# Kernel tuning notes

Measured on AMD Instinct MI355X. Metric: run time of the kernel, lower is better.

The kernel has to match this reference:

```python
import jax, jax.numpy as jnp
import numpy as np
import math

N_EMBD = 1024
N_HEAD = 16
HEAD_DIM = N_EMBD // N_HEAD


def setup_inputs() -> dict:
    key = jax.random.key(0)
    k_x, k_w1, k_b1, k_w2, k_b2 = jax.random.split(key, 5)
    B, T = 2, 2048
    x = jax.random.normal(k_x, (B, T, N_EMBD), dtype=jnp.float32)
    # ln1: Linear(n_embd, 3*n_embd); weights stored as [in, out] for x @ W
    W_qkv = jax.random.normal(k_w1, (N_EMBD, 3 * N_EMBD), dtype=jnp.float32) * 0.02
    b_qkv = jax.random.normal(k_b1, (3 * N_EMBD,), dtype=jnp.float32) * 0.02
    # ln2: Linear(n_embd, n_embd)
    W_out = jax.random.normal(k_w2, (N_EMBD, N_EMBD), dtype=jnp.float32) * 0.02
    b_out = jax.random.normal(k_b2, (N_EMBD,), dtype=jnp.float32) * 0.02
    return {"x": x, "W_qkv": W_qkv, "b_qkv": b_qkv, "W_out": W_out, "b_out": b_out}


def reference(x, W_qkv, b_qkv, W_out, b_out):
    B, T, C = x.shape
    qkv = x @ W_qkv + b_qkv                      # [B,T,3C]
    q, k, v = jnp.split(qkv, 3, axis=-1)
    # reshape to heads: [B, H, T, D]
    def to_heads(t):
        return t.reshape(B, T, N_HEAD, HEAD_DIM).transpose(0, 2, 1, 3)
    Q, K, V = to_heads(q), to_heads(k), to_heads(v)
    # NOTE: scale is 1/sqrt(n_head), as in the source (not sqrt(head_dim));
    # NOTE: no causal mask is applied, faithfully matching the source forward.
    scale = 1.0 / math.sqrt(N_HEAD)
    scores = jnp.einsum('bhqd,bhkd->bhqk', Q, K) * scale  # [B,H,T,T]
    attn = jax.nn.softmax(scores, axis=-1)
    out = jnp.einsum('bhqk,bhkd->bhqd', attn, V)          # [B,H,T,D]
    out = out.transpose(0, 2, 1, 3).reshape(B, T, C)
    # dropout = 0.0 -> identity (eval mode)
    return out @ W_out + b_out
```

## Files before the change

kernel.cpp:

```cpp
#include <hip/hip_runtime.h>
#include <hip/hip_bf16.h>
#include <stdint.h>

typedef __bf16 bf16_t;
typedef __bf16 bf16x8 __attribute__((ext_vector_type(8)));
typedef float  f32x4  __attribute__((ext_vector_type(4)));

#define AS1 __attribute__((address_space(1)))
#define AS3 __attribute__((address_space(3)))

__device__ __forceinline__ void gload16(const bf16_t* g, char* l) {
  __builtin_amdgcn_global_load_lds((AS1 const void*)(uintptr_t)g, (AS3 void*)l, 16, 0, 0);
}
__device__ __forceinline__ int swz8(int r) { return (r & 7) ^ ((r >> 2) & 6); }

#define C2S 0.36067376022224085f

__global__ __launch_bounds__(256) void prep(
    const float* __restrict__ x, const float* __restrict__ Wqkv, const float* __restrict__ Wout,
    bf16_t* __restrict__ xb, bf16_t* __restrict__ wqkvT, bf16_t* __restrict__ woutT) {
  __shared__ float tile[32][33];
  const int bid = blockIdx.x, tid = threadIdx.x;
  if (bid < 4096) {
    const int i = bid * 256 + tid;
    float4 v = reinterpret_cast<const float4*>(x)[i];
    union { bf16_t h[4]; unsigned long long u; } r;
    r.h[0] = (bf16_t)v.x; r.h[1] = (bf16_t)v.y; r.h[2] = (bf16_t)v.z; r.h[3] = (bf16_t)v.w;
    reinterpret_cast<unsigned long long*>(xb)[i] = r.u;
    return;
  }
  const float* W; bf16_t* Wt; int N, tb;
  if (bid < 7168) { W = Wqkv; Wt = wqkvT; N = 3072; tb = bid - 4096; }
  else            { W = Wout; Wt = woutT; N = 1024; tb = bid - 7168; }
  const int kb = (tb & 31) * 32, nb = (tb >> 5) * 32;
  const int tx = tid & 31, ty = tid >> 5;
#pragma unroll
  for (int i = 0; i < 32; i += 8)
    tile[ty + i][tx] = W[(size_t)(kb + ty + i) * N + nb + tx];
  __syncthreads();
#pragma unroll
  for (int i = 0; i < 32; i += 8)
    Wt[(size_t)(nb + ty + i) * 1024 + kb + tx] = (bf16_t)tile[tx][ty + i];
}

template<int MI>
__global__ __launch_bounds__(256) void gemm_bt(
    const bf16_t* __restrict__ A, const bf16_t* __restrict__ Bt,
    const float* __restrict__ bias,
    bf16_t* __restrict__ outb, bf16_t* __restrict__ vtb, float* __restrict__ outf,
    int M, int N, int K, int ldo, int mode) {
  __shared__ bf16_t lA[3][MI * 1024];
  __shared__ bf16_t lB[3][4096];
  const int tid = threadIdx.x;
  const int wave = tid >> 6, lane = tid & 63;
  const int lr = lane & 15, lg = lane >> 4;
  const int ntiles = N >> 7;
  const int bid = (blockIdx.x & 7) * ((int)gridDim.x >> 3) + (blockIdx.x >> 3);
  const int bn = bid % ntiles, bm = bid / ntiles;
  const int m0 = bm * (MI * 32), n0 = bn * 128;
  const int wr = wave >> 1, wc = wave & 1;
  f32x4 acc[MI][4] = {};

  auto stageg = [&](int buf, int k0) {
#pragma unroll
    for (int it = 0; it < MI / 2; ++it) {
      const int wbase = it * 256 + wave * 64;
      const int lam = wbase + lane;
      const int row = lam >> 2;
      const int colb = ((lam & 3) << 4) ^ (((row >> 1) & 3) << 4);
      gload16(A + (size_t)(m0 + row) * K + k0 + (colb >> 1), (char*)&lA[buf][0] + wbase * 16);
    }
#pragma unroll
    for (int it = 0; it < 2; ++it) {
      const int wbase = it * 256 + wave * 64;
      const int lam = wbase + lane;
      const int row = lam >> 2;
      const int colb = ((lam & 3) << 4) ^ (((row >> 1) & 3) << 4);
      gload16(Bt + (size_t)(n0 + row) * K + k0 + (colb >> 1), (char*)&lB[buf][0] + wbase * 16);
    }
  };

  const int nt = K >> 5;
  stageg(0, 0);
  stageg(1, 32);
  int cur = 0, stg = 2;

  for (int t = 0; t < nt; ++t) {
    if (t + 2 < nt) stageg(stg, (t + 2) << 5);
    if (t + 2 < nt) {
      if constexpr (MI == 4) asm volatile("s_waitcnt vmcnt(8)" ::: "memory");
      else                   asm volatile("s_waitcnt vmcnt(6)" ::: "memory");
    } else if (t + 1 < nt) {
      if constexpr (MI == 4) asm volatile("s_waitcnt vmcnt(4)" ::: "memory");
      else                   asm volatile("s_waitcnt vmcnt(3)" ::: "memory");
    } else {
      asm volatile("s_waitcnt vmcnt(0)" ::: "memory");
    }
    __builtin_amdgcn_s_barrier();
    __builtin_amdgcn_sched_barrier(0);

    const char* pA = (const char*)&lA[cur][0];
    const char* pB = (const char*)&lB[cur][0];
    bf16x8 af[MI], bfv[4];
#pragma unroll
    for (int mi = 0; mi < MI; ++mi) {
      const int row = wr * (MI * 16) + mi * 16 + lr;
      af[mi] = *reinterpret_cast<const bf16x8*>(
          pA + row * 64 + ((lg * 16) ^ (((row >> 1) & 3) << 4)));
    }
#pragma unroll
    for (int ni = 0; ni < 4; ++ni) {
      const int row = wc * 64 + ni * 16 + lr;
      bfv[ni] = *reinterpret_cast<const bf16x8*>(
          pB + row * 64 + ((lg * 16) ^ (((row >> 1) & 3) << 4)));
    }
    __builtin_amdgcn_s_setprio(1);
#pragma unroll
    for (int mi = 0; mi < MI; ++mi)
#pragma unroll
      for (int ni = 0; ni < 4; ++ni)
        acc[mi][ni] = __builtin_amdgcn_mfma_f32_16x16x32_bf16(af[mi], bfv[ni], acc[mi][ni], 0, 0, 0);
    __builtin_amdgcn_s_setprio(0);

    __builtin_amdgcn_sched_barrier(0);
    __builtin_amdgcn_s_barrier();
    cur = cur == 2 ? 0 : cur + 1;
    stg = stg == 2 ? 0 : stg + 1;
  }

#pragma unroll
  for (int mi = 0; mi < MI; ++mi) {
#pragma unroll
    for (int ni = 0; ni < 4; ++ni) {
      const int col = n0 + wc * 64 + ni * 16 + lr;
      const float bv = bias[col];
      const int rg0 = m0 + wr * (MI * 16) + mi * 16 + lg * 4;
      if (mode == 1 && col >= 2048) {
        const int colv = col - 2048;
        const int dd = colv & 63, hh = colv >> 6;
        const int bb = rg0 >> 11, t = rg0 & 2047;
        union { bf16_t h4[4]; unsigned long long u; } pk;
#pragma unroll
        for (int r = 0; r < 4; ++r) pk.h4[r] = (bf16_t)(acc[mi][ni][r] + bv);
        *reinterpret_cast<unsigned long long*>(
            vtb + (size_t)(bb * 16 + hh) * 131072 + (size_t)dd * 2048 + t) = pk.u;
      } else {
        const float sc = (mode == 1 && col < 1024) ? C2S : 1.f;
#pragma unroll
        for (int r = 0; r < 4; ++r) {
          const float v = (acc[mi][ni][r] + bv) * sc;
          if (mode == 2) outf[(size_t)(rg0 + r) * ldo + col] = v;
          else           outb[(size_t)(rg0 + r) * ldo + col] = (bf16_t)v;
        }
      }
    }
  }
}

__global__ __launch_bounds__(512) void attn_fwd(
    const bf16_t* __restrict__ qkv2,
    const bf16_t* __restrict__ vT,
    bf16_t* __restrict__ a0, bf16_t* __restrict__ a1,
    float* __restrict__ lbuf) {
  __shared__ bf16_t lds[3][8192];
  const int tid = threadIdx.x;
  const int wave = tid >> 6, lane = tid & 63;
  const int lr = lane & 15, lg = lane >> 4;
  const int id = blockIdx.x;
  const int xcd = id & 7, slot = id >> 3;
  const int bh = xcd * 4 + (slot & 3);
  const int rest = slot >> 2;
  const int qb = rest & 7, kvh = rest >> 3;
  const int b = bh >> 4, h = bh & 15;

  const int q0 = qb * 256 + wave * 32;
  const bf16_t* Qp = qkv2 + (size_t)(b * 2048 + q0) * 2048 + h * 64;
  bf16x8 qf[2][2];
#pragma unroll
  for (int hx = 0; hx < 2; ++hx) {
    qf[hx][0] = *reinterpret_cast<const bf16x8*>(Qp + (size_t)(hx * 16 + lr) * 2048 + lg * 8);
    qf[hx][1] = *reinterpret_cast<const bf16x8*>(Qp + (size_t)(hx * 16 + lr) * 2048 + 32 + lg * 8);
  }

  const int kr = tid >> 3;
  const int ks = (tid & 7) ^ swz8(kr);
  const bf16_t* Ksrc = qkv2 + (size_t)(b * 2048 + kvh * 1024 + kr) * 2048 + 1024 + h * 64 + ks * 8;
  const bf16_t* Vsrc = vT + (size_t)bh * 131072 + (size_t)kr * 2048 + kvh * 1024 + ks * 8;

  auto stage = [&](int buf, int kb) {
    char* base = (char*)&lds[buf][0] + wave * 1024;
    gload16(Ksrc + (size_t)kb * 131072, base);
    gload16(Vsrc + (size_t)kb * 64, base + 8192);
  };

  int kofs[4][2], vofs[4][2];
#pragma unroll
  for (int t = 0; t < 4; ++t) {
    const int kk = 32 * (t >> 1) + 8 * (lr >> 2) + 4 * (t & 1) + (lr & 3);
    const int sw = swz8(kk) << 4;
    kofs[t][0] = (kk << 7) + ((lg * 16) ^ sw);
    kofs[t][1] = (kk << 7) + ((64 + lg * 16) ^ sw);
  }
#pragma unroll
  for (int nc = 0; nc < 4; ++nc) {
    const int vr = nc * 16 + lr;
    const int sw = swz8(vr) << 4;
    vofs[nc][0] = 8192 + (vr << 7) + ((lg * 16) ^ sw);
    vofs[nc][1] = 8192 + (vr << 7) + ((64 + lg * 16) ^ sw);
  }

  f32x4 acc[2][4] = {};
  f32x4 accl[2] = {};
  bf16x8 ones;
#pragma unroll
  for (int j = 0; j < 8; ++j) ones[j] = (bf16_t)1.0f;

  stage(0, 0);
  stage(1, 1);
  int cur = 0, stg = 2;

  for (int kb = 0; kb < 16; ++kb) {
    if (kb + 2 < 16) stage(stg, kb + 2);
    if (kb + 2 < 16)      asm volatile("s_waitcnt vmcnt(4)" ::: "memory");
    else if (kb + 1 < 16) asm volatile("s_waitcnt vmcnt(2)" ::: "memory");
    else                  asm volatile("s_waitcnt vmcnt(0)" ::: "memory");
    __builtin_amdgcn_s_barrier();
    __builtin_amdgcn_sched_barrier(0);
    const char* bK = (const char*)&lds[cur][0];

    f32x4 s[2][4];
#pragma unroll
    for (int t = 0; t < 4; ++t) {
      const bf16x8 k0 = *reinterpret_cast<const bf16x8*>(bK + kofs[t][0]);
      const bf16x8 k1 = *reinterpret_cast<const bf16x8*>(bK + kofs[t][1]);
#pragma unroll
      for (int hx = 0; hx < 2; ++hx) {
        f32x4 z = {0.f, 0.f, 0.f, 0.f};
        z = __builtin_amdgcn_mfma_f32_16x16x32_bf16(k0, qf[hx][0], z, 0, 0, 0);
        s[hx][t] = __builtin_amdgcn_mfma_f32_16x16x32_bf16(k1, qf[hx][1], z, 0, 0, 0);
      }
    }

    bf16x8 pa[2][2];
#pragma unroll
    for (int hx = 0; hx < 2; ++hx) {
      float p[16];
#pragma unroll
      for (int t = 0; t < 4; ++t)
#pragma unroll
        for (int r = 0; r < 4; ++r)
          p[t * 4 + r] = __builtin_amdgcn_exp2f(s[hx][t][r]);
#pragma unroll
      for (int j = 0; j < 8; ++j) { pa[hx][0][j] = (bf16_t)p[j]; pa[hx][1][j] = (bf16_t)p[8 + j]; }
    }

    __builtin_amdgcn_s_setprio(1);
#pragma unroll
    for (int hx = 0; hx < 2; ++hx) {
      accl[hx] = __builtin_amdgcn_mfma_f32_16x16x32_bf16(pa[hx][0], ones, accl[hx], 0, 0, 0);
      accl[hx] = __builtin_amdgcn_mfma_f32_16x16x32_bf16(pa[hx][1], ones, accl[hx], 0, 0, 0);
    }

#pragma unroll
    for (int nc = 0; nc < 4; ++nc) {
      const bf16x8 v0 = *reinterpret_cast<const bf16x8*>(bK + vofs[nc][0]);
      const bf16x8 v1 = *reinterpret_cast<const bf16x8*>(bK + vofs[nc][1]);
#pragma unroll
      for (int hx = 0; hx < 2; ++hx) {
        acc[hx][nc] = __builtin_amdgcn_mfma_f32_16x16x32_bf16(pa[hx][0], v0, acc[hx][nc], 0, 0, 0);
        acc[hx][nc] = __builtin_amdgcn_mfma_f32_16x16x32_bf16(pa[hx][1], v1, acc[hx][nc], 0, 0, 0);
      }
    }
    __builtin_amdgcn_s_setprio(0);

    __builtin_amdgcn_sched_barrier(0);
    __builtin_amdgcn_s_barrier();
    cur = cur == 2 ? 0 : cur + 1;
    stg = stg == 2 ? 0 : stg + 1;
  }

  bf16_t* ap = kvh ? a1 : a0;
#pragma unroll
  for (int hx = 0; hx < 2; ++hx) {
#pragma unroll
    for (int r = 0; r < 4; ++r) {
      const float lf = 1.f / accl[hx][r];
      const int qg = q0 + hx * 16 + lg * 4 + r;
      bf16_t* op = ap + (size_t)(b * 2048 + qg) * 1024 + h * 64 + lr;
#pragma unroll
      for (int nc = 0; nc < 4; ++nc) op[nc * 16] = (bf16_t)(acc[hx][nc][r] * lf);
      if (lr == 0)
        lbuf[(size_t)(kvh * 4096 + b * 2048 + qg) * 16 + h] = accl[hx][r];
    }
  }
}

__global__ void attn_reduce(const bf16_t* __restrict__ a0, const bf16_t* __restrict__ a1,
                            const float* __restrict__ lbuf, bf16_t* __restrict__ aout) {
  const int i = blockIdx.x * 256 + threadIdx.x;
  const int r = i >> 7, h = (i & 127) >> 3;
  const float l0 = lbuf[(size_t)r * 16 + h];
  const float l1 = lbuf[(size_t)(4096 + r) * 16 + h];
  const float inv = 1.f / (l0 + l1);
  const float w0 = l0 * inv, w1 = l1 * inv;
  const bf16x8 v0 = reinterpret_cast<const bf16x8*>(a0)[i];
  const bf16x8 v1 = reinterpret_cast<const bf16x8*>(a1)[i];
  bf16x8 o;
#pragma unroll
  for (int j = 0; j < 8; ++j) o[j] = (bf16_t)(w0 * (float)v0[j] + w1 * (float)v1[j]);
  reinterpret_cast<bf16x8*>(aout)[i] = o;
}

extern "C" void kernel_launch(void* const* d_in, const int* in_sizes, int n_in,
                              void* d_out, int out_size, void* d_ws, size_t ws_size,
                              hipStream_t stream) {
  (void)in_sizes; (void)n_in; (void)out_size; (void)ws_size;
  const float* x    = (const float*)d_in[0];
  const float* Wqkv = (const float*)d_in[1];
  const float* bqkv = (const float*)d_in[2];
  const float* Wout = (const float*)d_in[3];
  const float* bout = (const float*)d_in[4];
  float* out = (float*)d_out;

  char* ws = (char*)d_ws;
  bf16_t* xb    = (bf16_t*)(ws);
  bf16_t* a0    = (bf16_t*)(ws);
  bf16_t* wqkvT = (bf16_t*)(ws + 8388608);
  bf16_t* woutT = (bf16_t*)(ws + 14680064);
  bf16_t* qkv2  = (bf16_t*)(ws + 16777216);
  bf16_t* aout  = (bf16_t*)(ws + 16777216);
  bf16_t* vT    = (bf16_t*)(ws + 33554432);
  bf16_t* a1    = (bf16_t*)(ws + 41943040);
  float*  lbuf  = (float*)(ws + 50331648);

  prep<<<8192, 256, 0, stream>>>(x, Wqkv, Wout, xb, wqkvT, woutT);
  gemm_bt<4><<<768, 256, 0, stream>>>(xb, wqkvT, bqkv, qkv2, vT, nullptr, 4096, 3072, 1024, 2048, 1);
  attn_fwd<<<512, 512, 0, stream>>>(qkv2, vT, a0, a1, lbuf);
  attn_reduce<<<2048, 256, 0, stream>>>(a0, a1, lbuf, aout);
  gemm_bt<2><<<512, 256, 0, stream>>>(aout, woutT, bout, nullptr, nullptr, out, 4096, 1024, 1024, 1024, 2);
}
```

Measured before the change: 113.9 us.

## Interleave GEMM LDS reads, global prefetch and MFMA in barrier-separated phases

Restructures the GEMM main loop into phases. Each phase issues a few LDS fragment reads and one slice of the next-tile global-to-LDS prefetch, then a barrier and lgkmcnt wait, then a batch of MFMAs. The aim is to overlap LDS traffic and global loads with matrix math instead of issuing all prefetches and reads ahead of the compute block. The vmcnt waits are adjusted to the new issue order, and more barriers per k-step are added, which adds synchronisation overhead and risks stalls.

```diff
diff --git a/kernel.cpp b/kernel.cpp
--- a/kernel.cpp
+++ b/kernel.cpp
@@ -15,6 +15,8 @@
 __device__ __forceinline__ int swz8(int r) { return (r & 7) ^ ((r >> 2) & 6); }
 
 #define C2S 0.36067376022224085f
+#define LGKM0 do { asm volatile("s_waitcnt lgkmcnt(0)" ::: "memory"); \
+                   __builtin_amdgcn_sched_barrier(0); } while (0)
 
 __global__ __launch_bounds__(256) void prep(
     const float* __restrict__ x, const float* __restrict__ Wqkv, const float* __restrict__ Wout,
@@ -61,23 +63,30 @@
   const int wr = wave >> 1, wc = wave & 1;
   f32x4 acc[MI][4] = {};
 
+  const int lamw = wave * 64 + lane;
+  const int srow = lamw >> 2;
+  const int scolb = ((lamw & 3) << 4) ^ (((srow >> 1) & 3) << 4);
+  auto stageA = [&](int buf, int k0, int it) {
+    gload16(A + (size_t)(m0 + it * 64 + srow) * K + k0 + (scolb >> 1),
+            (char*)&lA[buf][0] + (it * 256 + wave * 64) * 16);
+  };
+  auto stageB = [&](int buf, int k0, int it) {
+    gload16(Bt + (size_t)(n0 + it * 64 + srow) * K + k0 + (scolb >> 1),
+            (char*)&lB[buf][0] + (it * 256 + wave * 64) * 16);
+  };
   auto stageg = [&](int buf, int k0) {
 #pragma unroll
-    for (int it = 0; it < MI / 2; ++it) {
-      const int wbase = it * 256 + wave * 64;
-      const int lam = wbase + lane;
-      const int row = lam >> 2;
-      const int colb = ((lam & 3) << 4) ^ (((row >> 1) & 3) << 4);
-      gload16(A + (size_t)(m0 + row) * K + k0 + (colb >> 1), (char*)&lA[buf][0] + wbase * 16);
-    }
-#pragma unroll
-    for (int it = 0; it < 2; ++it) {
-      const int wbase = it * 256 + wave * 64;
-      const int lam = wbase + lane;
-      const int row = lam >> 2;
-      const int colb = ((lam & 3) << 4) ^ (((row >> 1) & 3) << 4);
-      gload16(Bt + (size_t)(n0 + row) * K + k0 + (colb >> 1), (char*)&lB[buf][0] + wbase * 16);
-    }
+    for (int it = 0; it < MI / 2; ++it) stageA(buf, k0, it);
+    stageB(buf, k0, 0); stageB(buf, k0, 1);
+  };
+
+  auto ldA = [&](const char* p, int mi) {
+    const int row = wr * (MI * 16) + mi * 16 + lr;
+    return *reinterpret_cast<const bf16x8*>(p + row * 64 + ((lg * 16) ^ (((row >> 1) & 3) << 4)));
+  };
+  auto ldB = [&](const char* p, int ni) {
+    const int row = wc * 64 + ni * 16 + lr;
+    return *reinterpret_cast<const bf16x8*>(p + row * 64 + ((lg * 16) ^ (((row >> 1) & 3) << 4)));
   };
 
   const int nt = K >> 5;
@@ -86,11 +95,7 @@
   int cur = 0, stg = 2;
 
   for (int t = 0; t < nt; ++t) {
-    if (t + 2 < nt) stageg(stg, (t + 2) << 5);
-    if (t + 2 < nt) {
-      if constexpr (MI == 4) asm volatile("s_waitcnt vmcnt(8)" ::: "memory");
-      else                   asm volatile("s_waitcnt vmcnt(6)" ::: "memory");
-    } else if (t + 1 < nt) {
+    if (t + 1 < nt) {
       if constexpr (MI == 4) asm volatile("s_waitcnt vmcnt(4)" ::: "memory");
       else                   asm volatile("s_waitcnt vmcnt(3)" ::: "memory");
     } else {
@@ -101,29 +106,69 @@
 
     const char* pA = (const char*)&lA[cur][0];
     const char* pB = (const char*)&lB[cur][0];
+    const bool pf = (t + 2 < nt);
+    const int k2 = (t + 2) << 5;
     bf16x8 af[MI], bfv[4];
-#pragma unroll
-    for (int mi = 0; mi < MI; ++mi) {
-      const int row = wr * (MI * 16) + mi * 16 + lr;
-      af[mi] = *reinterpret_cast<const bf16x8*>(
-          pA + row * 64 + ((lg * 16) ^ (((row >> 1) & 3) << 4)));
-    }
-#pragma unroll
-    for (int ni = 0; ni < 4; ++ni) {
-      const int row = wc * 64 + ni * 16 + lr;
-      bfv[ni] = *reinterpret_cast<const bf16x8*>(
-          pB + row * 64 + ((lg * 16) ^ (((row >> 1) & 3) << 4)));
-    }
-    __builtin_amdgcn_s_setprio(1);
-#pragma unroll
-    for (int mi = 0; mi < MI; ++mi)
-#pragma unroll
-      for (int ni = 0; ni < 4; ++ni)
-        acc[mi][ni] = __builtin_amdgcn_mfma_f32_16x16x32_bf16(af[mi], bfv[ni], acc[mi][ni], 0, 0, 0);
-    __builtin_amdgcn_s_setprio(0);
-
-    __builtin_amdgcn_sched_barrier(0);
-    __builtin_amdgcn_s_barrier();
+
+    if constexpr (MI == 4) {
+      af[0] = ldA(pA, 0); af[1] = ldA(pA, 1);
+      bfv[0] = ldB(pB, 0); bfv[1] = ldB(pB, 1);
+      if (pf) stageA(stg, k2, 0);
+      __builtin_amdgcn_s_barrier(); LGKM0;
+      __builtin_amdgcn_s_setprio(1);
+      acc[0][0] = __builtin_amdgcn_mfma_f32_16x16x32_bf16(af[0], bfv[0], acc[0][0], 0, 0, 0);
+      acc[0][1] = __builtin_amdgcn_mfma_f32_16x16x32_bf16(af[0], bfv[1], acc[0][1], 0, 0, 0);
+      acc[1][0] = __builtin_amdgcn_mfma_f32_16x16x32_bf16(af[1], bfv[0], acc[1][0], 0, 0, 0);
+      acc[1][1] = __builtin_amdgcn_mfma_f32_16x16x32_bf16(af[1], bfv[1], acc[1][1], 0, 0, 0);
+      __builtin_amdgcn_s_setprio(0);
+      bfv[2] = ldB(pB, 2); bfv[3] = ldB(pB, 3);
+      if (pf) stageA(stg, k2, 1);
+      __builtin_amdgcn_s_barrier(); LGKM0;
+      __builtin_amdgcn_s_setprio(1);
+      acc[0][2] = __builtin_amdgcn_mfma_f32_16x16x32_bf16(af[0], bfv[2], acc[0][2], 0, 0, 0);
+      acc[0][3] = __builtin_amdgcn_mfma_f32_16x16x32_bf16(af[0], bfv[3], acc[0][3], 0, 0, 0);
+      acc[1][2] = __builtin_amdgcn_mfma_f32_16x16x32_bf16(af[1], bfv[2], acc[1][2], 0, 0, 0);
+      acc[1][3] = __builtin_amdgcn_mfma_f32_16x16x32_bf16(af[1], bfv[3], acc[1][3], 0, 0, 0);
+      __builtin_amdgcn_s_setprio(0);
+      af[2] = ldA(pA, 2); af[3] = ldA(pA, 3);
+      if (pf) stageB(stg, k2, 0);
+      __builtin_amdgcn_s_barrier(); LGKM0;
+      __builtin_amdgcn_s_setprio(1);
+      acc[2][0] = __builtin_amdgcn_mfma_f32_16x16x32_bf16(af[2], bfv[0], acc[2][0], 0, 0, 0);
+      acc[2][1] = __builtin_amdgcn_mfma_f32_16x16x32_bf16(af[2], bfv[1], acc[2][1], 0, 0, 0);
+      acc[3][0] = __builtin_amdgcn_mfma_f32_16x16x32_bf16(af[3], bfv[0], acc[3][0], 0, 0, 0);
+      acc[3][1] = __builtin_amdgcn_mfma_f32_16x16x32_bf16(af[3], bfv[1], acc[3][1], 0, 0, 0);
+      __builtin_amdgcn_s_setprio(0);
+      if (pf) stageB(stg, k2, 1);
+      __builtin_amdgcn_s_barrier();
+      __builtin_amdgcn_s_setprio(1);
+      acc[2][2] = __builtin_amdgcn_mfma_f32_16x16x32_bf16(af[2], bfv[2], acc[2][2], 0, 0, 0);
+      acc[2][3] = __builtin_amdgcn_mfma_f32_16x16x32_bf16(af[2], bfv[3], acc[2][3], 0, 0, 0);
+      acc[3][2] = __builtin_amdgcn_mfma_f32_16x16x32_bf16(af[3], bfv[2], acc[3][2], 0, 0, 0);
+      acc[3][3] = __builtin_amdgcn_mfma_f32_16x16x32_bf16(af[3], bfv[3], acc[3][3], 0, 0, 0);
+      __builtin_amdgcn_s_setprio(0);
+    } else {
+      af[0] = ldA(pA, 0); af[1] = ldA(pA, 1);
+      bfv[0] = ldB(pB, 0); bfv[1] = ldB(pB, 1);
+      if (pf) { stageA(stg, k2, 0); stageB(stg, k2, 0); }
+      __builtin_amdgcn_s_barrier(); LGKM0;
+      __builtin_amdgcn_s_setprio(1);
+      acc[0][0] = __builtin_amdgcn_mfma_f32_16x16x32_bf16(af[0], bfv[0], acc[0][0], 0, 0, 0);
+      acc[0][1] = __builtin_amdgcn_mfma_f32_16x16x32_bf16(af[0], bfv[1], acc[0][1], 0, 0, 0);
+      acc[1][0] = __builtin_amdgcn_mfma_f32_16x16x32_bf16(af[1], bfv[0], acc[1][0], 0, 0, 0);
+      acc[1][1] = __builtin_amdgcn_mfma_f32_16x16x32_bf16(af[1], bfv[1], acc[1][1], 0, 0, 0);
+      __builtin_amdgcn_s_setprio(0);
+      bfv[2] = ldB(pB, 2); bfv[3] = ldB(pB, 3);
+      if (pf) stageB(stg, k2, 1);
+      __builtin_amdgcn_s_barrier(); LGKM0;
+      __builtin_amdgcn_s_setprio(1);
+      acc[0][2] = __builtin_amdgcn_mfma_f32_16x16x32_bf16(af[0], bfv[2], acc[0][2], 0, 0, 0);
+      acc[0][3] = __builtin_amdgcn_mfma_f32_16x16x32_bf16(af[0], bfv[3], acc[0][3], 0, 0, 0);
+      acc[1][2] = __builtin_amdgcn_mfma_f32_16x16x32_bf16(af[1], bfv[2], acc[1][2], 0, 0, 0);
+      acc[1][3] = __builtin_amdgcn_mfma_f32_16x16x32_bf16(af[1], bfv[3], acc[1][3], 0, 0, 0);
+      __builtin_amdgcn_s_setprio(0);
+    }
+
     cur = cur == 2 ? 0 : cur + 1;
     stg = stg == 2 ? 0 : stg + 1;
   }
@@ -260,7 +305,6 @@
       accl[hx] = __builtin_amdgcn_mfma_f32_16x16x32_bf16(pa[hx][0], ones, accl[hx], 0, 0, 0);
       accl[hx] = __builtin_amdgcn_mfma_f32_16x16x32_bf16(pa[hx][1], ones, accl[hx], 0, 0, 0);
     }
-
 #pragma unroll
     for (int nc = 0; nc < 4; ++nc) {
       const bf16x8 v0 = *reinterpret_cast<const bf16x8*>(bK + vofs[nc][0]);
```

Result: no change. 114.2 us (+0.3%).
